# Kernel optimization log

Hardware: AMD Instinct MI355X
Metric: run time of the kernel (lower is better)

## Reference

```python
import jax, jax.numpy as jnp
import numpy as np

N = 4096       # graph nodes (= image batch)
FIN = 2048     # resnet50 feature dim
HD = 256       # hidden_dim
C = 10         # num_classes
THRESH = 0.05  # cosine-sim threshold for adjacency
ATTN_SLOPE = 0.2   # DGL GATConv leaky-relu slope
MLP_SLOPE = 0.01   # F.leaky_relu default slope


def setup_inputs() -> dict:
    key = jax.random.key(0)
    ks = jax.random.split(key, 24)
    g = lambda k, shp, s=0.05: (jax.random.normal(k, shp, jnp.float32) * s)
    inp = {
        "x": jax.random.normal(ks[0], (N, FIN), jnp.float32),
        # GAT layer 1: 2048 -> 256, 4 heads, linear residual
        "W0": g(ks[1], (FIN, 4 * HD)),
        "al0": g(ks[2], (4, HD)), "ar0": g(ks[3], (4, HD)),
        "b0": jnp.zeros((4 * HD,), jnp.float32),
        "R0": g(ks[4], (FIN, 4 * HD)),
        # GAT mid layer: 256 -> 256, 4 heads, linear residual
        "W1": g(ks[5], (HD, 4 * HD)),
        "al1": g(ks[6], (4, HD)), "ar1": g(ks[7], (4, HD)),
        "b1": jnp.zeros((4 * HD,), jnp.float32),
        "R1": g(ks[8], (HD, 4 * HD)),
        # GAT final layer: 256 -> 256, 1 head, identity residual
        "W2": g(ks[9], (HD, HD)),
        "al2": g(ks[10], (1, HD)), "ar2": g(ks[11], (1, HD)),
        "b2": jnp.zeros((HD,), jnp.float32),
        # heads
        "Wl1": g(ks[12], (FIN + HD, 1024)), "bl1": jnp.zeros((1024,), jnp.float32),
        "Wc1": g(ks[13], (1024, C)), "bc1": jnp.zeros((C,), jnp.float32),
        "Wc2": g(ks[14], (FIN, C)), "bc2": jnp.zeros((C,), jnp.float32),
    }
    return inp


def _gat(h, mask, W, al, ar, b, R):
    """DGL GATConv with residual=True, masked dense edge-softmax.
    h: [N, Fin]; mask: [N, N] bool (mask[dst, src]); returns [N, H, Fout]."""
    n = h.shape[0]
    H, F = al.shape
    feat = (h @ W).reshape(n, H, F)                      # [N, H, F] src/dst projections
    el = jnp.einsum('nhf,hf->nh', feat, al)              # src score
    er = jnp.einsum('nhf,hf->nh', feat, ar)              # dst score
    e = er[:, None, :] + el[None, :, :]                  # [dst, src, H]
    e = jnp.where(e > 0, e, ATTN_SLOPE * e)              # leaky relu
    e = jnp.where(mask[:, :, None], e, -jnp.inf)
    alpha = jax.nn.softmax(e, axis=1)                    # edge softmax over src
    rst = jnp.einsum('dsh,shf->dhf', alpha, feat)        # aggregate
    res = (h @ R).reshape(n, H, F) if R is not None else h.reshape(n, -1, F)
    return rst + res + b.reshape(1, H, F)


def reference(x, W0, al0, ar0, b0, R0, W1, al1, ar1, b1, R1,
              W2, al2, ar2, b2, Wl1, bl1, Wc1, bc1, Wc2, bc2):
    # dynamic threshold graph from cosine similarity
    xn = x / jnp.linalg.norm(x, axis=1, keepdims=True)
    mask = (xn @ xn.T) > THRESH                          # symmetric, includes self-loops
    # stacked GAT layers, heads summed
    h = jax.nn.relu(_gat(x, mask, W0, al0, ar0, b0, R0).sum(axis=1))
    h = jax.nn.relu(_gat(h, mask, W1, al1, ar1, b1, R1).sum(axis=1))
    h = _gat(h, mask, W2, al2, ar2, b2, None).sum(axis=1)  # last layer: no relu
    # MLP heads
    z = jnp.concatenate([x, h], axis=1)                  # [N, 2048+256]
    z = jax.nn.leaky_relu(z @ Wl1 + bl1, MLP_SLOPE)
    logits_1 = z @ Wc1 + bc1
    logits_2 = x @ Wc2 + bc2
    return logits_1, logits_2
```

## Files before the change

kernel.cpp:

```cpp
#include <hip/hip_runtime.h>
#include <cstdint>
#include <cstddef>

#define NNODE 4096
#define FIND  2048
#define HD_   256
#define NC_   10
#define THRESH_ 0.05f
#define LOG2E_ 1.4426950408889634f

typedef unsigned long long u64;
typedef __attribute__((ext_vector_type(8))) short bf16x8;
typedef __attribute__((ext_vector_type(4))) float f32x4;

__device__ inline unsigned short f2bf_rne(float f){
  unsigned u = __builtin_bit_cast(unsigned, f);
  unsigned r = u + 0x7FFFu + ((u >> 16) & 1u);
  return (unsigned short)(r >> 16);
}
__device__ inline float bf2f(unsigned short h){
  unsigned u = ((unsigned)h) << 16;
  return __builtin_bit_cast(float, u);
}
__device__ __forceinline__ float fexp2(float x){ return __builtin_amdgcn_exp2f(x); }

__device__ __forceinline__ void gld16(const void* g, void* l){
  __builtin_amdgcn_global_load_lds(
      (const __attribute__((address_space(1))) unsigned int*)g,
      (__attribute__((address_space(3))) unsigned int*)l, 16, 0, 0);
}

__global__ void rownorm_bf(const float* __restrict__ x,
                           unsigned short* __restrict__ oh, unsigned short* __restrict__ ol){
  int row = blockIdx.x; int t = threadIdx.x;
  const float4* xr = reinterpret_cast<const float4*>(x + (size_t)row*FIND);
  float s = 0.f;
  #pragma unroll
  for (int i = 0; i < FIND/4/256; ++i){
    float4 v = xr[t + i*256];
    s += v.x*v.x + v.y*v.y + v.z*v.z + v.w*v.w;
  }
  #pragma unroll
  for (int o = 32; o > 0; o >>= 1) s += __shfl_down(s, o);
  __shared__ float red[4];
  __shared__ float invn;
  if ((t & 63) == 0) red[t >> 6] = s;
  __syncthreads();
  if (t == 0) invn = rsqrtf(red[0] + red[1] + red[2] + red[3]);
  __syncthreads();
  float inv = invn;
  #pragma unroll
  for (int i = 0; i < FIND/4/256; ++i){
    float4 v = xr[t + i*256];
    float a[4] = {v.x*inv, v.y*inv, v.z*inv, v.w*inv};
    ushort4 hv, lv;
    unsigned short* hp = &hv.x; unsigned short* lp = &lv.x;
    #pragma unroll
    for (int j = 0; j < 4; ++j){
      unsigned short h = f2bf_rne(a[j]);
      hp[j] = h; lp[j] = f2bf_rne(a[j] - bf2f(h));
    }
    size_t off = (size_t)row*FIND + (t + i*256)*4;
    *reinterpret_cast<ushort4*>(oh + off) = hv;
    *reinterpret_cast<ushort4*>(ol + off) = lv;
  }
}

__global__ void f2bf_k(const float* __restrict__ in, unsigned short* __restrict__ oh,
                       unsigned short* __restrict__ ol, int n4){
  int idx = blockIdx.x*256 + threadIdx.x;
  if (idx >= n4) return;
  float4 v = reinterpret_cast<const float4*>(in)[idx];
  float a[4] = {v.x, v.y, v.z, v.w};
  ushort4 hv, lv;
  unsigned short* hp = &hv.x; unsigned short* lp = &lv.x;
  #pragma unroll
  for (int j = 0; j < 4; ++j){
    unsigned short h = f2bf_rne(a[j]);
    hp[j] = h; lp[j] = f2bf_rne(a[j] - bf2f(h));
  }
  reinterpret_cast<ushort4*>(oh)[idx] = hv;
  reinterpret_cast<ushort4*>(ol)[idx] = lv;
}

template<int H>
__global__ void foldT_k(const float* __restrict__ R, unsigned short* __restrict__ oh,
                        unsigned short* __restrict__ ol, int K, int F, int ktiles){
  int bid = blockIdx.x;
  int f0 = (bid / ktiles) * 64, k0 = (bid % ktiles) * 64;
  __shared__ float tile[64][65];
  int t = threadIdx.x;
  {
    int tf = t & 63, tk4 = t >> 6;
    #pragma unroll
    for (int m = 0; m < 16; ++m){
      int kl = tk4 + m*4;
      float s = 0.f;
      #pragma unroll
      for (int h = 0; h < H; ++h)
        s += R[(size_t)(k0 + kl)*(H*F) + h*F + f0 + tf];
      tile[kl][tf] = s;
    }
  }
  __syncthreads();
  {
    int tk = t & 63, tf4 = t >> 6;
    #pragma unroll
    for (int m = 0; m < 16; ++m){
      int fl = tf4 + m*4;
      float s = tile[tk][fl];
      unsigned short hv = f2bf_rne(s);
      size_t o = (size_t)(f0 + fl)*K + k0 + tk;
      oh[o] = hv;
      ol[o] = f2bf_rne(s - bf2f(hv));
    }
  }
}

__global__ void bfold_k(const float* __restrict__ b, float* __restrict__ out, int H, int F){
  int f = threadIdx.x;
  if (f < F){
    float s = 0.f;
    for (int h = 0; h < H; ++h) s += b[h*F + f];
    out[f] = s;
  }
}

__global__ void mega_gemm(const unsigned short* __restrict__ XNh, const unsigned short* __restrict__ XNl,
                          const unsigned short* __restrict__ Xh,  const unsigned short* __restrict__ Xl,
                          const unsigned short* __restrict__ W0h, const unsigned short* __restrict__ W0l,
                          const unsigned short* __restrict__ WLh, const unsigned short* __restrict__ WLl,
                          float* __restrict__ FT, unsigned short* __restrict__ FTB,
                          float* __restrict__ Z1, u64* __restrict__ Mk){
  __shared__ unsigned short smem[4*128*32];
  unsigned short* sAh = smem;
  unsigned short* sAl = smem + 4096;
  unsigned short* sBh = smem + 8192;
  unsigned short* sBl = smem + 12288;
  const int t = threadIdx.x, lane = t & 63, w = t >> 6;
  const int wr = w >> 1, wc = w & 1, l15 = lane & 15, lg = lane >> 4;

  int nwg = gridDim.x, bid = blockIdx.x;
  int wg = (bid & 7)*(nwg >> 3) + (bid >> 3);

  int role, brow, bcol;
  const unsigned short *Ah, *Al, *Bh, *Bl;
  float* C = nullptr; int ldc = 0; size_t ldb;
  if (wg < 528){
    role = 0;
    int rem = wg, i = 0;
    while (rem >= 32 - i){ rem -= 32 - i; ++i; }
    brow = i; bcol = i + rem;
    Ah = XNh; Al = XNl; Bh = XNh; Bl = XNl; ldb = FIND;
  } else if (wg < 848){
    role = 1;
    int l = wg - 528; brow = l / 10; bcol = l % 10;
    Ah = Xh; Al = Xl; Bh = W0h; Bl = W0l; ldb = FIND;
    C = FT; ldc = 1280;
  } else {
    role = 2;
    int l = wg - 848; brow = l >> 3; bcol = l & 7;
    Ah = Xh; Al = Xl; Bh = WLh; Bl = WLl; ldb = 2304;
    C = Z1; ldc = 1024;
  }
  const int row0 = brow*128, col0 = bcol*128;

  const int c0 = 2*w, c1 = 2*w + 1;
  const int rsub = lane >> 2, piece = lane & 3;
  const size_t ld2a = (size_t)FIND*2, ld2b = ldb*2;
  const size_t a0 = (size_t)(row0 + 16*c0 + rsub)*ld2a + piece*16;
  const size_t a1 = (size_t)(row0 + 16*c1 + rsub)*ld2a + piece*16;
  const size_t b0 = (size_t)(col0 + 16*c0 + rsub)*ld2b + piece*16;
  const size_t b1 = (size_t)(col0 + 16*c1 + rsub)*ld2b + piece*16;
  const char* pA0h = (const char*)Ah + a0;  const char* pA1h = (const char*)Ah + a1;
  const char* pA0l = (const char*)Al + a0;  const char* pA1l = (const char*)Al + a1;
  const char* pB0h = (const char*)Bh + b0;  const char* pB1h = (const char*)Bh + b1;
  const char* pB0l = (const char*)Bl + b0;  const char* pB1l = (const char*)Bl + b1;
  char* lA0h = (char*)sAh + c0*1024;  char* lA1h = (char*)sAh + c1*1024;
  char* lA0l = (char*)sAl + c0*1024;  char* lA1l = (char*)sAl + c1*1024;
  char* lB0h = (char*)sBh + c0*1024;  char* lB1h = (char*)sBh + c1*1024;
  char* lB0l = (char*)sBl + c0*1024;  char* lB1l = (char*)sBl + c1*1024;

  f32x4 acc[4][4] = {};
  for (int kt = 0; kt < 64; ++kt){
    __syncthreads();
    gld16(pA0h, lA0h); gld16(pA1h, lA1h);
    gld16(pA0l, lA0l); gld16(pA1l, lA1l);
    gld16(pB0h, lB0h); gld16(pB1h, lB1h);
    gld16(pB0l, lB0l); gld16(pB1l, lB1l);
    pA0h += 64; pA1h += 64; pA0l += 64; pA1l += 64;
    pB0h += 64; pB1h += 64; pB0l += 64; pB1l += 64;
    __syncthreads();
    bf16x8 fb_h[4], fb_l[4];
    #pragma unroll
    for (int j = 0; j < 4; ++j){
      int bo = (wc*64 + j*16 + l15)*32 + lg*8;
      fb_h[j] = *reinterpret_cast<const bf16x8*>(sBh + bo);
      fb_l[j] = *reinterpret_cast<const bf16x8*>(sBl + bo);
    }
    #pragma unroll
    for (int i = 0; i < 4; ++i){
      int ao = (wr*64 + i*16 + l15)*32 + lg*8;
      bf16x8 fah = *reinterpret_cast<const bf16x8*>(sAh + ao);
      bf16x8 fal = *reinterpret_cast<const bf16x8*>(sAl + ao);
      #pragma unroll
      for (int j = 0; j < 4; ++j){
        acc[i][j] = __builtin_amdgcn_mfma_f32_16x16x32_bf16(fah, fb_h[j], acc[i][j], 0, 0, 0);
        acc[i][j] = __builtin_amdgcn_mfma_f32_16x16x32_bf16(fah, fb_l[j], acc[i][j], 0, 0, 0);
        acc[i][j] = __builtin_amdgcn_mfma_f32_16x16x32_bf16(fal, fb_h[j], acc[i][j], 0, 0, 0);
      }
    }
  }

  if (role == 0){
    #pragma unroll
    for (int i = 0; i < 4; ++i){
      #pragma unroll
      for (int r = 0; r < 4; ++r){
        u64 bits = 0ull;
        #pragma unroll
        for (int j = 0; j < 4; ++j)
          if (acc[i][j][r] > THRESH_) bits |= 1ull << (j*16 + l15);
        #pragma unroll
        for (int m = 1; m <= 8; m <<= 1) bits |= __shfl_xor(bits, m);
        if (l15 == 0){
          int gr = row0 + wr*64 + i*16 + lg*4 + r;
          Mk[(size_t)gr*64 + (col0 >> 6) + wc] = bits;
        }
      }
    }
    if (row0 != col0){
      #pragma unroll
      for (int j = 0; j < 4; ++j){
        u64 tb = 0ull;
        #pragma unroll
        for (int i = 0; i < 4; ++i)
          #pragma unroll
          for (int r = 0; r < 4; ++r)
            if (acc[i][j][r] > THRESH_) tb |= 1ull << (i*16 + lg*4 + r);
        tb |= __shfl_xor(tb, 16);
        tb |= __shfl_xor(tb, 32);
        if (lg == 0){
          int gc = col0 + wc*64 + j*16 + l15;
          Mk[(size_t)gc*64 + (row0 >> 6) + wr] = tb;
        }
      }
    }
  } else {
    #pragma unroll
    for (int i = 0; i < 4; ++i){
      int gr = row0 + wr*64 + i*16 + lg*4;
      #pragma unroll
      for (int j = 0; j < 4; ++j){
        int gc = col0 + wc*64 + j*16 + l15;
        #pragma unroll
        for (int r = 0; r < 4; ++r){
          float v = acc[i][j][r];
          C[(size_t)(gr + r)*ldc + gc] = v;
          if (role == 1) FTB[(size_t)(gr + r)*1280 + gc] = f2bf_rne(v);
        }
      }
    }
  }
}

template<int EPI>
__global__ void gemm_bf(const unsigned short* __restrict__ Ah, const unsigned short* __restrict__ Al,
                        const unsigned short* __restrict__ Bh, const unsigned short* __restrict__ Bl,
                        float* __restrict__ C, unsigned short* __restrict__ Cb,
                        int K, int lda, int ldb, int ldc, int gridx,
                        const float* __restrict__ bias, float param){
  __shared__ unsigned short smem[4*128*32];
  unsigned short* sAh = smem;
  unsigned short* sAl = smem + 4096;
  unsigned short* sBh = smem + 8192;
  unsigned short* sBl = smem + 12288;
  const int t = threadIdx.x, lane = t & 63, w = t >> 6;
  const int wr = w >> 1, wc = w & 1, l15 = lane & 15, lg = lane >> 4;

  int nwg = gridDim.x, bid = blockIdx.x;
  int wg = ((nwg & 7) == 0) ? ((bid & 7)*(nwg >> 3) + (bid >> 3)) : bid;
  int brow = wg / gridx, bcol = wg % gridx;
  const int row0 = brow*128, col0 = bcol*128;

  const int c0 = 2*w, c1 = 2*w + 1;
  const int rsub = lane >> 2, piece = lane & 3;
  const size_t ld2a = (size_t)lda*2, ld2b = (size_t)ldb*2;
  const size_t a0 = (size_t)(row0 + 16*c0 + rsub)*ld2a + piece*16;
  const size_t a1 = (size_t)(row0 + 16*c1 + rsub)*ld2a + piece*16;
  const size_t b0 = (size_t)(col0 + 16*c0 + rsub)*ld2b + piece*16;
  const size_t b1 = (size_t)(col0 + 16*c1 + rsub)*ld2b + piece*16;
  const char* pA0h = (const char*)Ah + a0;  const char* pA1h = (const char*)Ah + a1;
  const char* pA0l = (const char*)Al + a0;  const char* pA1l = (const char*)Al + a1;
  const char* pB0h = (const char*)Bh + b0;  const char* pB1h = (const char*)Bh + b1;
  const char* pB0l = (const char*)Bl + b0;  const char* pB1l = (const char*)Bl + b1;
  char* lA0h = (char*)sAh + c0*1024;  char* lA1h = (char*)sAh + c1*1024;
  char* lA0l = (char*)sAl + c0*1024;  char* lA1l = (char*)sAl + c1*1024;
  char* lB0h = (char*)sBh + c0*1024;  char* lB1h = (char*)sBh + c1*1024;
  char* lB0l = (char*)sBl + c0*1024;  char* lB1l = (char*)sBl + c1*1024;

  f32x4 acc[4][4] = {};
  const int nk = K >> 5;
  for (int kt = 0; kt < nk; ++kt){
    __syncthreads();
    gld16(pA0h, lA0h); gld16(pA1h, lA1h);
    gld16(pA0l, lA0l); gld16(pA1l, lA1l);
    gld16(pB0h, lB0h); gld16(pB1h, lB1h);
    gld16(pB0l, lB0l); gld16(pB1l, lB1l);
    pA0h += 64; pA1h += 64; pA0l += 64; pA1l += 64;
    pB0h += 64; pB1h += 64; pB0l += 64; pB1l += 64;
    __syncthreads();
    bf16x8 fb_h[4], fb_l[4];
    #pragma unroll
    for (int j = 0; j < 4; ++j){
      int bo = (wc*64 + j*16 + l15)*32 + lg*8;
      fb_h[j] = *reinterpret_cast<const bf16x8*>(sBh + bo);
      fb_l[j] = *reinterpret_cast<const bf16x8*>(sBl + bo);
    }
    #pragma unroll
    for (int i = 0; i < 4; ++i){
      int ao = (wr*64 + i*16 + l15)*32 + lg*8;
      bf16x8 fah = *reinterpret_cast<const bf16x8*>(sAh + ao);
      bf16x8 fal = *reinterpret_cast<const bf16x8*>(sAl + ao);
      #pragma unroll
      for (int j = 0; j < 4; ++j){
        acc[i][j] = __builtin_amdgcn_mfma_f32_16x16x32_bf16(fah, fb_h[j], acc[i][j], 0, 0, 0);
        acc[i][j] = __builtin_amdgcn_mfma_f32_16x16x32_bf16(fah, fb_l[j], acc[i][j], 0, 0, 0);
        acc[i][j] = __builtin_amdgcn_mfma_f32_16x16x32_bf16(fal, fb_h[j], acc[i][j], 0, 0, 0);
      }
    }
  }

  #pragma unroll
  for (int i = 0; i < 4; ++i){
    int gr = row0 + wr*64 + i*16 + lg*4;
    #pragma unroll
    for (int j = 0; j < 4; ++j){
      int gc = col0 + wc*64 + j*16 + l15;
      #pragma unroll
      for (int r = 0; r < 4; ++r){
        float v = acc[i][j][r];
        size_t o = (size_t)(gr + r)*ldc + gc;
        if (EPI == 3){
          v += C[o] + bias[gc];
          v = v > 0.f ? v : param*v;
        }
        C[o] = v;
        if (EPI == 0 && Cb) Cb[o] = f2bf_rne(v);
      }
    }
  }
}

template<int H>
__global__ void el_er_k(const float* __restrict__ feat, int ldf,
                        const float* __restrict__ al, const float* __restrict__ ar,
                        float* __restrict__ el2, float* __restrict__ er2){
  int n = blockIdx.x, t = threadIdx.x;
  __shared__ float red[8];
  #pragma unroll
  for (int h = 0; h < H; ++h){
    float v = feat[(size_t)n*ldf + h*HD_ + t];
    float a = v * al[h*HD_ + t];
    float b = v * ar[h*HD_ + t];
    #pragma unroll
    for (int o = 32; o > 0; o >>= 1){ a += __shfl_down(a, o); b += __shfl_down(b, o); }
    if ((t & 63) == 0){ red[t >> 6] = a; red[4 + (t >> 6)] = b; }
    __syncthreads();
    if (t == 0){
      el2[n*H + h] = (red[0] + red[1] + red[2] + red[3]) * LOG2E_;
      er2[n*H + h] = (red[4] + red[5] + red[6] + red[7]) * LOG2E_;
    }
    __syncthreads();
  }
}

template<int H>
__global__ void elmax_k(const float* __restrict__ el2, float* __restrict__ out){
  int h = blockIdx.x, t = threadIdx.x;
  float m = -1e30f;
  for (int n = t; n < NNODE; n += 256) m = fmaxf(m, el2[(size_t)n*H + h]);
  #pragma unroll
  for (int o = 32; o > 0; o >>= 1) m = fmaxf(m, __shfl_down(m, o));
  __shared__ float red[4];
  if ((t & 63) == 0) red[t >> 6] = m;
  __syncthreads();
  if (t == 0) out[h] = fmaxf(fmaxf(red[0], red[1]), fmaxf(red[2], red[3]));
}

template<int H, bool RELU, bool OUTF32>
__global__ void sagg_k(const unsigned short* __restrict__ FTB, int ldf,
                       const u64* __restrict__ Mk,
                       const float* __restrict__ el2, const float* __restrict__ er2,
                       const float* __restrict__ melg2,
                       const float* __restrict__ res, int ldres,
                       const float* __restrict__ bias,
                       float* __restrict__ outf,
                       unsigned short* __restrict__ oh, unsigned short* __restrict__ ol){
  int d = blockIdx.x, t = threadIdx.x;
  const int g = t >> 6, q = t & 63;
  const int h = (H == 4) ? g : 0;
  const int wlo = (H == 1) ? g*16 : 0;
  const int whi = (H == 1) ? wlo + 16 : 64;
  const float er2d = er2[(size_t)d*H + h];
  const float sub = er2d + melg2[h];
  const float m2 = fmaxf(sub, 0.2f*sub);
  const unsigned short* fb = FTB + 4*q + ((H == 4) ? 256*g : 0);
  float4 acc = {0.f, 0.f, 0.f, 0.f};
  float sm = 0.f;
  for (int wdi = wlo; wdi < whi; ++wdi){
    u64 bits = Mk[(size_t)d*64 + wdi];
    while (bits){
      int b = __builtin_ctzll(bits);
      bits &= bits - 1ull;
      int s = wdi*64 + b;
      float sc = er2d + el2[(size_t)s*H + h];
      sc = fmaxf(sc, 0.2f*sc);
      float wt = fexp2(sc - m2);
      sm += wt;
      ushort4 v = *reinterpret_cast<const ushort4*>(fb + (size_t)s*ldf);
      acc.x += wt*bf2f(v.x); acc.y += wt*bf2f(v.y);
      acc.z += wt*bf2f(v.z); acc.w += wt*bf2f(v.w);
    }
  }
  __shared__ float lred[4][256];
  __shared__ float lsm[4];
  if (H == 4){
    float inv = 1.f / sm;
    acc.x *= inv; acc.y *= inv; acc.z *= inv; acc.w *= inv;
  } else if (q == 0){
    lsm[g] = sm;
  }
  lred[g][q*4+0] = acc.x; lred[g][q*4+1] = acc.y;
  lred[g][q*4+2] = acc.z; lred[g][q*4+3] = acc.w;
  __syncthreads();
  float v = ((lred[0][t] + lred[1][t]) + lred[2][t]) + lred[3][t];
  if (H == 1) v /= (lsm[0] + lsm[1]) + (lsm[2] + lsm[3]);
  v += res[(size_t)d*ldres + t] + bias[t];
  if (RELU) v = fmaxf(v, 0.f);
  if (OUTF32) outf[(size_t)d*HD_ + t] = v;
  unsigned short hv = f2bf_rne(v);
  oh[(size_t)d*HD_ + t] = hv;
  ol[(size_t)d*HD_ + t] = f2bf_rne(v - bf2f(hv));
}

__global__ void head_k(const float* __restrict__ A, int K, const float* __restrict__ W,
                       const float* __restrict__ b, float* __restrict__ out){
  int row = blockIdx.x, t = threadIdx.x;
  float p[NC_];
  #pragma unroll
  for (int j = 0; j < NC_; ++j) p[j] = 0.f;
  for (int k = t; k < K; k += 256){
    float a = A[(size_t)row*K + k];
    #pragma unroll
    for (int j = 0; j < NC_; ++j) p[j] += a * W[k*NC_ + j];
  }
  #pragma unroll
  for (int j = 0; j < NC_; ++j){
    #pragma unroll
    for (int o = 32; o > 0; o >>= 1) p[j] += __shfl_down(p[j], o);
  }
  __shared__ float red[4][NC_];
  if ((t & 63) == 0){
    #pragma unroll
    for (int j = 0; j < NC_; ++j) red[t >> 6][j] = p[j];
  }
  __syncthreads();
  if (t < NC_)
    out[(size_t)row*NC_ + t] = red[0][t] + red[1][t] + red[2][t] + red[3][t] + b[t];
}

extern "C" void kernel_launch(void* const* d_in, const int* in_sizes, int n_in,
                              void* d_out, int out_size, void* d_ws, size_t ws_size,
                              hipStream_t stream){
  const float* x   = (const float*)d_in[0];
  const float* W0  = (const float*)d_in[1];
  const float* al0 = (const float*)d_in[2];
  const float* ar0 = (const float*)d_in[3];
  const float* b0  = (const float*)d_in[4];
  const float* R0  = (const float*)d_in[5];
  const float* W1  = (const float*)d_in[6];
  const float* al1 = (const float*)d_in[7];
  const float* ar1 = (const float*)d_in[8];
  const float* b1  = (const float*)d_in[9];
  const float* R1  = (const float*)d_in[10];
  const float* W2  = (const float*)d_in[11];
  const float* al2 = (const float*)d_in[12];
  const float* ar2 = (const float*)d_in[13];
  const float* b2  = (const float*)d_in[14];
  const float* Wl1 = (const float*)d_in[15];
  const float* bl1 = (const float*)d_in[16];
  const float* Wc1 = (const float*)d_in[17];
  const float* bc1 = (const float*)d_in[18];
  const float* Wc2 = (const float*)d_in[19];
  const float* bc2 = (const float*)d_in[20];
  (void)in_sizes; (void)n_in; (void)out_size; (void)ws_size;

  char* ws = (char*)d_ws;
  size_t off = 0;
  auto alloc = [&](size_t bytes)->char*{
    char* p = ws + off; off += (bytes + 255) & ~(size_t)255; return p;
  };
  typedef unsigned short us;
  u64* MASK = (u64*)alloc((size_t)NNODE*64*8);
  us* W0h = (us*)alloc((size_t)1280*2048*2);  us* W0l = (us*)alloc((size_t)1280*2048*2);
  us* W1h = (us*)alloc((size_t)1280*256*2);   us* W1l = (us*)alloc((size_t)1280*256*2);
  us* W2h = (us*)alloc((size_t)256*256*2);    us* W2l = (us*)alloc((size_t)256*256*2);
  us* WLh = (us*)alloc((size_t)1024*2304*2);  us* WLl = (us*)alloc((size_t)1024*2304*2);
  float* BF0 = (float*)alloc(256*4);
  float* BF1 = (float*)alloc(256*4);
  float* EL2 = (float*)alloc((size_t)NNODE*4*4);
  float* ER2 = (float*)alloc((size_t)NNODE*4*4);
  float* MELG = (float*)alloc(4*4);
  us* XNh = (us*)alloc((size_t)NNODE*FIND*2);
  us* XNl = (us*)alloc((size_t)NNODE*FIND*2);
  us* Xh  = (us*)alloc((size_t)NNODE*FIND*2);
  us* Xl  = (us*)alloc((size_t)NNODE*FIND*2);
  float* FT = (float*)alloc((size_t)NNODE*1280*4);
  us* FTB = (us*)alloc((size_t)NNODE*1280*2);
  float* H2 = (float*)alloc((size_t)NNODE*HD_*4);
  us* H1h = (us*)alloc((size_t)NNODE*HD_*2);  us* H1l = (us*)alloc((size_t)NNODE*HD_*2);
  us* H2h = (us*)alloc((size_t)NNODE*HD_*2);  us* H2l = (us*)alloc((size_t)NNODE*HD_*2);
  us* H3h = (us*)alloc((size_t)NNODE*HD_*2);  us* H3l = (us*)alloc((size_t)NNODE*HD_*2);
  float* Z1 = (float*)alloc((size_t)NNODE*1024*4);

  float* out1 = (float*)d_out;
  float* out2 = out1 + (size_t)NNODE*NC_;

  foldT_k<1><<<512, 256, 0, stream>>>(W0, W0h, W0l, 2048, 1024, 32);
  foldT_k<4><<<128, 256, 0, stream>>>(R0, W0h + (size_t)1024*2048, W0l + (size_t)1024*2048, 2048, 256, 32);
  foldT_k<1><<< 64, 256, 0, stream>>>(W1, W1h, W1l, 256, 1024, 4);
  foldT_k<4><<< 16, 256, 0, stream>>>(R1, W1h + (size_t)1024*256, W1l + (size_t)1024*256, 256, 256, 4);
  foldT_k<1><<< 16, 256, 0, stream>>>(W2, W2h, W2l, 256, 256, 4);
  foldT_k<1><<<576, 256, 0, stream>>>(Wl1, WLh, WLl, 2304, 1024, 36);
  bfold_k<<<1, 256, 0, stream>>>(b0, BF0, 4, 256);
  bfold_k<<<1, 256, 0, stream>>>(b1, BF1, 4, 256);
  f2bf_k<<<(NNODE*FIND/4+255)/256, 256, 0, stream>>>(x, Xh, Xl, NNODE*FIND/4);
  rownorm_bf<<<NNODE, 256, 0, stream>>>(x, XNh, XNl);

  mega_gemm<<<1104, 256, 0, stream>>>(XNh, XNl, Xh, Xl, W0h, W0l, WLh, WLl, FT, FTB, Z1, MASK);

  el_er_k<4><<<NNODE, 256, 0, stream>>>(FT, 1280, al0, ar0, EL2, ER2);
  elmax_k<4><<<4, 256, 0, stream>>>(EL2, MELG);
  sagg_k<4,true,false><<<NNODE, 256, 0, stream>>>(FTB, 1280, MASK, EL2, ER2, MELG,
      FT + 1024, 1280, BF0, nullptr, H1h, H1l);

  gemm_bf<0><<<320, 256, 0, stream>>>(H1h, H1l, W1h, W1l, FT, FTB,
      256, 256, 256, 1280, 10, nullptr, 0.f);
  el_er_k<4><<<NNODE, 256, 0, stream>>>(FT, 1280, al1, ar1, EL2, ER2);
  elmax_k<4><<<4, 256, 0, stream>>>(EL2, MELG);
  sagg_k<4,true,true><<<NNODE, 256, 0, stream>>>(FTB, 1280, MASK, EL2, ER2, MELG,
      FT + 1024, 1280, BF1, H2, H2h, H2l);

  gemm_bf<0><<<64, 256, 0, stream>>>(H2h, H2l, W2h, W2l, FT, FTB,
      256, 256, 256, 256, 2, nullptr, 0.f);
  el_er_k<1><<<NNODE, 256, 0, stream>>>(FT, 256, al2, ar2, EL2, ER2);
  elmax_k<1><<<1, 256, 0, stream>>>(EL2, MELG);
  sagg_k<1,false,false><<<NNODE, 256, 0, stream>>>(FTB, 256, MASK, EL2, ER2, MELG,
      H2, 256, b2, nullptr, H3h, H3l);

  gemm_bf<3><<<256, 256, 0, stream>>>(H3h, H3l, WLh + 2048, WLl + 2048, Z1, nullptr,
      256, 256, 2304, 1024, 8, bl1, 0.01f);

  head_k<<<NNODE, 256, 0, stream>>>(Z1, 1024, Wc1, bc1, out1);
  head_k<<<NNODE, 256, 0, stream>>>(x, FIND, Wc2, bc2, out2);
}
```

Measured before the change: 578.6 us.

## Drop low-order bf16 split for activations in projection GEMMs; skip redundant fp32 stores

Activation operands in the feature and MLP GEMMs now use a single bf16 component instead of a high/low split, so those GEMMs issue two MFMAs per tile instead of three and load one fewer A tile. The cosine-similarity mask GEMM keeps the three-term split. The fp32 copy of projected features is now written only for the residual columns, and the attention-score kernels read the bf16 copy instead. This cuts MFMA work, memory traffic and LDS use, at the cost of lower precision in the activations.

Measured after the change: 571.8 us. Within noise of the previous version (-1.2%).

```diff
diff --git a/kernel.cpp b/kernel.cpp
--- a/kernel.cpp
+++ b/kernel.cpp
@@ -66,21 +66,14 @@
   }
 }
 
-__global__ void f2bf_k(const float* __restrict__ in, unsigned short* __restrict__ oh,
-                       unsigned short* __restrict__ ol, int n4){
+__global__ void f2bf1_k(const float* __restrict__ in, unsigned short* __restrict__ oh, int n4){
   int idx = blockIdx.x*256 + threadIdx.x;
   if (idx >= n4) return;
   float4 v = reinterpret_cast<const float4*>(in)[idx];
-  float a[4] = {v.x, v.y, v.z, v.w};
-  ushort4 hv, lv;
-  unsigned short* hp = &hv.x; unsigned short* lp = &lv.x;
-  #pragma unroll
-  for (int j = 0; j < 4; ++j){
-    unsigned short h = f2bf_rne(a[j]);
-    hp[j] = h; lp[j] = f2bf_rne(a[j] - bf2f(h));
-  }
+  ushort4 hv;
+  hv.x = f2bf_rne(v.x); hv.y = f2bf_rne(v.y);
+  hv.z = f2bf_rne(v.z); hv.w = f2bf_rne(v.w);
   reinterpret_cast<ushort4*>(oh)[idx] = hv;
-  reinterpret_cast<ushort4*>(ol)[idx] = lv;
 }
 
 template<int H>
@@ -127,7 +120,7 @@
 }
 
 __global__ void mega_gemm(const unsigned short* __restrict__ XNh, const unsigned short* __restrict__ XNl,
-                          const unsigned short* __restrict__ Xh,  const unsigned short* __restrict__ Xl,
+                          const unsigned short* __restrict__ Xh,
                           const unsigned short* __restrict__ W0h, const unsigned short* __restrict__ W0l,
                           const unsigned short* __restrict__ WLh, const unsigned short* __restrict__ WLl,
                           float* __restrict__ FT, unsigned short* __restrict__ FTB,
@@ -144,7 +137,7 @@
   int wg = (bid & 7)*(nwg >> 3) + (bid >> 3);
 
   int role, brow, bcol;
-  const unsigned short *Ah, *Al, *Bh, *Bl;
+  const unsigned short *Ah, *Al = nullptr, *Bh, *Bl;
   float* C = nullptr; int ldc = 0; size_t ldb;
   if (wg < 528){
     role = 0;
@@ -155,14 +148,15 @@
   } else if (wg < 848){
     role = 1;
     int l = wg - 528; brow = l / 10; bcol = l % 10;
-    Ah = Xh; Al = Xl; Bh = W0h; Bl = W0l; ldb = FIND;
+    Ah = Xh; Bh = W0h; Bl = W0l; ldb = FIND;
     C = FT; ldc = 1280;
   } else {
     role = 2;
     int l = wg - 848; brow = l >> 3; bcol = l & 7;
-    Ah = Xh; Al = Xl; Bh = WLh; Bl = WLl; ldb = 2304;
+    Ah = Xh; Bh = WLh; Bl = WLl; ldb = 2304;
     C = Z1; ldc = 1024;
   }
+  const bool three = (role == 0);
   const int row0 = brow*128, col0 = bcol*128;
 
   const int c0 = 2*w, c1 = 2*w + 1;
@@ -173,7 +167,8 @@
   const size_t b0 = (size_t)(col0 + 16*c0 + rsub)*ld2b + piece*16;
   const size_t b1 = (size_t)(col0 + 16*c1 + rsub)*ld2b + piece*16;
   const char* pA0h = (const char*)Ah + a0;  const char* pA1h = (const char*)Ah + a1;
-  const char* pA0l = (const char*)Al + a0;  const char* pA1l = (const char*)Al + a1;
+  const char* pA0l = three ? (const char*)Al + a0 : nullptr;
+  const char* pA1l = three ? (const char*)Al + a1 : nullptr;
   const char* pB0h = (const char*)Bh + b0;  const char* pB1h = (const char*)Bh + b1;
   const char* pB0l = (const char*)Bl + b0;  const char* pB1l = (const char*)Bl + b1;
   char* lA0h = (char*)sAh + c0*1024;  char* lA1h = (char*)sAh + c1*1024;
@@ -185,10 +180,13 @@
   for (int kt = 0; kt < 64; ++kt){
     __syncthreads();
     gld16(pA0h, lA0h); gld16(pA1h, lA1h);
-    gld16(pA0l, lA0l); gld16(pA1l, lA1l);
+    if (three){
+      gld16(pA0l, lA0l); gld16(pA1l, lA1l);
+      pA0l += 64; pA1l += 64;
+    }
     gld16(pB0h, lB0h); gld16(pB1h, lB1h);
     gld16(pB0l, lB0l); gld16(pB1l, lB1l);
-    pA0h += 64; pA1h += 64; pA0l += 64; pA1l += 64;
+    pA0h += 64; pA1h += 64;
     pB0h += 64; pB1h += 64; pB0l += 64; pB1l += 64;
     __syncthreads();
     bf16x8 fb_h[4], fb_l[4];
@@ -202,12 +200,16 @@
     for (int i = 0; i < 4; ++i){
       int ao = (wr*64 + i*16 + l15)*32 + lg*8;
       bf16x8 fah = *reinterpret_cast<const bf16x8*>(sAh + ao);
-      bf16x8 fal = *reinterpret_cast<const bf16x8*>(sAl + ao);
       #pragma unroll
       for (int j = 0; j < 4; ++j){
         acc[i][j] = __builtin_amdgcn_mfma_f32_16x16x32_bf16(fah, fb_h[j], acc[i][j], 0, 0, 0);
         acc[i][j] = __builtin_amdgcn_mfma_f32_16x16x32_bf16(fah, fb_l[j], acc[i][j], 0, 0, 0);
-        acc[i][j] = __builtin_amdgcn_mfma_f32_16x16x32_bf16(fal, fb_h[j], acc[i][j], 0, 0, 0);
+      }
+      if (three){
+        bf16x8 fal = *reinterpret_cast<const bf16x8*>(sAl + ao);
+        #pragma unroll
+        for (int j = 0; j < 4; ++j)
+          acc[i][j] = __builtin_amdgcn_mfma_f32_16x16x32_bf16(fal, fb_h[j], acc[i][j], 0, 0, 0);
       }
     }
   }
@@ -247,6 +249,7 @@
       }
     }
   } else {
+    const int f32min = (role == 1) ? 1024 : 0;
     #pragma unroll
     for (int i = 0; i < 4; ++i){
       int gr = row0 + wr*64 + i*16 + lg*4;
@@ -256,8 +259,8 @@
         #pragma unroll
         for (int r = 0; r < 4; ++r){
           float v = acc[i][j][r];
-          C[(size_t)(gr + r)*ldc + gc] = v;
           if (role == 1) FTB[(size_t)(gr + r)*1280 + gc] = f2bf_rne(v);
+          if (gc >= f32min) C[(size_t)(gr + r)*ldc + gc] = v;
         }
       }
     }
@@ -265,16 +268,15 @@
 }
 
 template<int EPI>
-__global__ void gemm_bf(const unsigned short* __restrict__ Ah, const unsigned short* __restrict__ Al,
+__global__ void gemm_bf(const unsigned short* __restrict__ Ah,
                         const unsigned short* __restrict__ Bh, const unsigned short* __restrict__ Bl,
                         float* __restrict__ C, unsigned short* __restrict__ Cb,
                         int K, int lda, int ldb, int ldc, int gridx,
-                        const float* __restrict__ bias, float param){
-  __shared__ unsigned short smem[4*128*32];
+                        const float* __restrict__ bias, float param, int f32min){
+  __shared__ unsigned short smem[3*128*32];
   unsigned short* sAh = smem;
-  unsigned short* sAl = smem + 4096;
-  unsigned short* sBh = smem + 8192;
-  unsigned short* sBl = smem + 12288;
+  unsigned short* sBh = smem + 4096;
+  unsigned short* sBl = smem + 8192;
   const int t = threadIdx.x, lane = t & 63, w = t >> 6;
   const int wr = w >> 1, wc = w & 1, l15 = lane & 15, lg = lane >> 4;
 
@@ -291,11 +293,9 @@
   const size_t b0 = (size_t)(col0 + 16*c0 + rsub)*ld2b + piece*16;
   const size_t b1 = (size_t)(col0 + 16*c1 + rsub)*ld2b + piece*16;
   const char* pA0h = (const char*)Ah + a0;  const char* pA1h = (const char*)Ah + a1;
-  const char* pA0l = (const char*)Al + a0;  const char* pA1l = (const char*)Al + a1;
   const char* pB0h = (const char*)Bh + b0;  const char* pB1h = (const char*)Bh + b1;
   const char* pB0l = (const char*)Bl + b0;  const char* pB1l = (const char*)Bl + b1;
   char* lA0h = (char*)sAh + c0*1024;  char* lA1h = (char*)sAh + c1*1024;
-  char* lA0l = (char*)sAl + c0*1024;  char* lA1l = (char*)sAl + c1*1024;
   char* lB0h = (char*)sBh + c0*1024;  char* lB1h = (char*)sBh + c1*1024;
   char* lB0l = (char*)sBl + c0*1024;  char* lB1l = (char*)sBl + c1*1024;
 
@@ -304,10 +304,9 @@
   for (int kt = 0; kt < nk; ++kt){
     __syncthreads();
     gld16(pA0h, lA0h); gld16(pA1h, lA1h);
-    gld16(pA0l, lA0l); gld16(pA1l, lA1l);
     gld16(pB0h, lB0h); gld16(pB1h, lB1h);
     gld16(pB0l, lB0l); gld16(pB1l, lB1l);
-    pA0h += 64; pA1h += 64; pA0l += 64; pA1l += 64;
+    pA0h += 64; pA1h += 64;
     pB0h += 64; pB1h += 64; pB0l += 64; pB1l += 64;
     __syncthreads();
     bf16x8 fb_h[4], fb_l[4];
@@ -321,12 +320,10 @@
     for (int i = 0; i < 4; ++i){
       int ao = (wr*64 + i*16 + l15)*32 + lg*8;
       bf16x8 fah = *reinterpret_cast<const bf16x8*>(sAh + ao);
-      bf16x8 fal = *reinterpret_cast<const bf16x8*>(sAl + ao);
       #pragma unroll
       for (int j = 0; j < 4; ++j){
         acc[i][j] = __builtin_amdgcn_mfma_f32_16x16x32_bf16(fah, fb_h[j], acc[i][j], 0, 0, 0);
         acc[i][j] = __builtin_amdgcn_mfma_f32_16x16x32_bf16(fah, fb_l[j], acc[i][j], 0, 0, 0);
-        acc[i][j] = __builtin_amdgcn_mfma_f32_16x16x32_bf16(fal, fb_h[j], acc[i][j], 0, 0, 0);
       }
     }
   }
@@ -344,23 +341,25 @@
         if (EPI == 3){
           v += C[o] + bias[gc];
           v = v > 0.f ? v : param*v;
+          C[o] = v;
+        } else {
+          if (Cb) Cb[o] = f2bf_rne(v);
+          if (gc >= f32min) C[o] = v;
         }
-        C[o] = v;
-        if (EPI == 0 && Cb) Cb[o] = f2bf_rne(v);
       }
     }
   }
 }
 
 template<int H>
-__global__ void el_er_k(const float* __restrict__ feat, int ldf,
+__global__ void el_er_k(const unsigned short* __restrict__ feat, int ldf,
                         const float* __restrict__ al, const float* __restrict__ ar,
                         float* __restrict__ el2, float* __restrict__ er2){
   int n = blockIdx.x, t = threadIdx.x;
   __shared__ float red[8];
   #pragma unroll
   for (int h = 0; h < H; ++h){
-    float v = feat[(size_t)n*ldf + h*HD_ + t];
+    float v = bf2f(feat[(size_t)n*ldf + h*HD_ + t]);
     float a = v * al[h*HD_ + t];
     float b = v * ar[h*HD_ + t];
     #pragma unroll
@@ -396,7 +395,7 @@
                        const float* __restrict__ res, int ldres,
                        const float* __restrict__ bias,
                        float* __restrict__ outf,
-                       unsigned short* __restrict__ oh, unsigned short* __restrict__ ol){
+                       unsigned short* __restrict__ oh){
   int d = blockIdx.x, t = threadIdx.x;
   const int g = t >> 6, q = t & 63;
   const int h = (H == 4) ? g : 0;
@@ -439,9 +438,7 @@
   v += res[(size_t)d*ldres + t] + bias[t];
   if (RELU) v = fmaxf(v, 0.f);
   if (OUTF32) outf[(size_t)d*HD_ + t] = v;
-  unsigned short hv = f2bf_rne(v);
-  oh[(size_t)d*HD_ + t] = hv;
-  ol[(size_t)d*HD_ + t] = f2bf_rne(v - bf2f(hv));
+  oh[(size_t)d*HD_ + t] = f2bf_rne(v);
 }
 
 __global__ void head_k(const float* __restrict__ A, int K, const float* __restrict__ W,
@@ -515,13 +512,12 @@
   us* XNh = (us*)alloc((size_t)NNODE*FIND*2);
   us* XNl = (us*)alloc((size_t)NNODE*FIND*2);
   us* Xh  = (us*)alloc((size_t)NNODE*FIND*2);
-  us* Xl  = (us*)alloc((size_t)NNODE*FIND*2);
   float* FT = (float*)alloc((size_t)NNODE*1280*4);
   us* FTB = (us*)alloc((size_t)NNODE*1280*2);
   float* H2 = (float*)alloc((size_t)NNODE*HD_*4);
-  us* H1h = (us*)alloc((size_t)NNODE*HD_*2);  us* H1l = (us*)alloc((size_t)NNODE*HD_*2);
-  us* H2h = (us*)alloc((size_t)NNODE*HD_*2);  us* H2l = (us*)alloc((size_t)NNODE*HD_*2);
-  us* H3h = (us*)alloc((size_t)NNODE*HD_*2);  us* H3l = (us*)alloc((size_t)NNODE*HD_*2);
+  us* H1h = (us*)alloc((size_t)NNODE*HD_*2);
+  us* H2h = (us*)alloc((size_t)NNODE*HD_*2);
+  us* H3h = (us*)alloc((size_t)NNODE*HD_*2);
   float* Z1 = (float*)alloc((size_t)NNODE*1024*4);
 
   float* out1 = (float*)d_out;
@@ -535,32 +531,32 @@
   foldT_k<1><<<576, 256, 0, stream>>>(Wl1, WLh, WLl, 2304, 1024, 36);
   bfold_k<<<1, 256, 0, stream>>>(b0, BF0, 4, 256);
   bfold_k<<<1, 256, 0, stream>>>(b1, BF1, 4, 256);
-  f2bf_k<<<(NNODE*FIND/4+255)/256, 256, 0, stream>>>(x, Xh, Xl, NNODE*FIND/4);
+  f2bf1_k<<<(NNODE*FIND/4+255)/256, 256, 0, stream>>>(x, Xh, NNODE*FIND/4);
   rownorm_bf<<<NNODE, 256, 0, stream>>>(x, XNh, XNl);
 
-  mega_gemm<<<1104, 256, 0, stream>>>(XNh, XNl, Xh, Xl, W0h, W0l, WLh, WLl, FT, FTB, Z1, MASK);
-
-  el_er_k<4><<<NNODE, 256, 0, stream>>>(FT, 1280, al0, ar0, EL2, ER2);
+  mega_gemm<<<1104, 256, 0, stream>>>(XNh, XNl, Xh, W0h, W0l, WLh, WLl, FT, FTB, Z1, MASK);
+
+  el_er_k<4><<<NNODE, 256, 0, stream>>>(FTB, 1280, al0, ar0, EL2, ER2);
   elmax_k<4><<<4, 256, 0, stream>>>(EL2, MELG);
   sagg_k<4,true,false><<<NNODE, 256, 0, stream>>>(FTB, 1280, MASK, EL2, ER2, MELG,
-      FT + 1024, 1280, BF0, nullptr, H1h, H1l);
-
-  gemm_bf<0><<<320, 256, 0, stream>>>(H1h, H1l, W1h, W1l, FT, FTB,
-      256, 256, 256, 1280, 10, nullptr, 0.f);
-  el_er_k<4><<<NNODE, 256, 0, stream>>>(FT, 1280, al1, ar1, EL2, ER2);
+      FT + 1024, 1280, BF0, nullptr, H1h);
+
+  gemm_bf<0><<<320, 256, 0, stream>>>(H1h, W1h, W1l, FT, FTB,
+      256, 256, 256, 1280, 10, nullptr, 0.f, 1024);
+  el_er_k<4><<<NNODE, 256, 0, stream>>>(FTB, 1280, al1, ar1, EL2, ER2);
   elmax_k<4><<<4, 256, 0, stream>>>(EL2, MELG);
   sagg_k<4,true,true><<<NNODE, 256, 0, stream>>>(FTB, 1280, MASK, EL2, ER2, MELG,
-      FT + 1024, 1280, BF1, H2, H2h, H2l);
-
-  gemm_bf<0><<<64, 256, 0, stream>>>(H2h, H2l, W2h, W2l, FT, FTB,
-      256, 256, 256, 256, 2, nullptr, 0.f);
-  el_er_k<1><<<NNODE, 256, 0, stream>>>(FT, 256, al2, ar2, EL2, ER2);
+      FT + 1024, 1280, BF1, H2, H2h);
+
+  gemm_bf<0><<<64, 256, 0, stream>>>(H2h, W2h, W2l, FT, FTB,
+      256, 256, 256, 256, 2, nullptr, 0.f, 1 << 30);
+  el_er_k<1><<<NNODE, 256, 0, stream>>>(FTB, 256, al2, ar2, EL2, ER2);
   elmax_k<1><<<1, 256, 0, stream>>>(EL2, MELG);
   sagg_k<1,false,false><<<NNODE, 256, 0, stream>>>(FTB, 256, MASK, EL2, ER2, MELG,
-      H2, 256, b2, nullptr, H3h, H3l);
-
-  gemm_bf<3><<<256, 256, 0, stream>>>(H3h, H3l, WLh + 2048, WLl + 2048, Z1, nullptr,
-      256, 256, 2304, 1024, 8, bl1, 0.01f);
+      H2, 256, b2, nullptr, H3h);
+
+  gemm_bf<3><<<256, 256, 0, stream>>>(H3h, WLh + 2048, WLl + 2048, Z1, nullptr,
+      256, 256, 2304, 1024, 8, bl1, 0.01f, 0);
 
   head_k<<<NNODE, 256, 0, stream>>>(Z1, 1024, Wc1, bc1, out1);
   head_k<<<NNODE, 256, 0, stream>>>(x, FIND, Wc2, bc2, out2);
```
